# Kernel tuning notes

Measured on AMD Instinct MI355X. Metric: run time of the kernel, lower is better.

Reference implementation:

```python
import jax, jax.numpy as jnp
import numpy as np

B, R, C = 256, 1024, 1024
N_IDX = 64


def setup_inputs() -> dict:
    key = jax.random.key(0)
    kx, = jax.random.split(key, 1)
    x = jax.random.normal(kx, (B, R, C), dtype=jnp.float32)
    rows = jnp.arange(N_IDX, dtype=jnp.int32)
    cols = jnp.arange(N_IDX, dtype=jnp.int32)
    return {"x": x, "rows": rows, "cols": cols}


def _mute_msb(x):
    # frexp: x = m * 2**e with m in [0.5, 1). Muting the MSB of the exponent
    # (per the original: e = 0 if e > 0 else e) multiplies x by 2**(min(e,0)-e),
    # i.e. scales by 2**(-e) when e > 0, identity otherwise.
    e = jnp.frexp(x)[1]                                   # int exponent
    e = jax.lax.stop_gradient(e)
    scale = jnp.where(e > 0, jnp.exp2(-e.astype(x.dtype)), jnp.ones_like(x))
    return x * scale


def reference(x, rows, cols):
    # Boolean mask over the [R, C] plane selecting the (rows x cols) grid.
    mask = jnp.zeros((x.shape[1], x.shape[2]), dtype=bool)
    mask = mask.at[rows[:, None], cols[None, :]].set(True)
    y = _mute_msb(x)
    # Apply only on the selected grid, broadcast over batch.
    return jnp.where(mask[None, :, :], y, x)
```

## Files before the change

### kernel.cpp

```cpp
#include <hip/hip_runtime.h>
#include <hip/hip_bf16.h>


#define RR 1024
#define CC 1024
#define UNROLL 4

typedef float f4 __attribute__((ext_vector_type(4)));

__global__ void build_masks_kernel(const int* __restrict__ rows,
                                   const int* __restrict__ cols,
                                   unsigned* __restrict__ masks,
                                   int nr, int nc) {
    int t = threadIdx.x;
    if (t < 64) masks[t] = 0u;
    __syncthreads();
    if (t < nr) {
        int r = rows[t];
        atomicOr(&masks[r >> 5], 1u << (r & 31));
    }
    if (t < nc) {
        int c = cols[t];
        atomicOr(&masks[32 + (c >> 5)], 1u << (c & 31));
    }
}

__device__ __forceinline__ void mute4(f4& v, unsigned m) {
#pragma unroll
    for (int k = 0; k < 4; ++k) {
        if ((m >> k) & 1u) {
            unsigned u = __float_as_uint(v[k]);
            unsigned E = (u >> 23) & 0xffu;
            if (E >= 127u && E < 255u)
                v[k] = __uint_as_float((u & 0x807fffffu) | (126u << 23));
        }
    }
}

__global__ void copy_mute_kernel(const f4* __restrict__ x,
                                 f4* __restrict__ out,
                                 const unsigned* __restrict__ masks,
                                 int nrows) {
    __shared__ unsigned rowmask[32];
    int tid = threadIdx.x;
    if (tid < 32) rowmask[tid] = masks[tid];
    __syncthreads();

    unsigned colword = masks[32 + (tid >> 3)];
    unsigned colnib = (colword >> ((tid & 7) * 4)) & 0xFu;

    int rowstride = gridDim.x * UNROLL;
    long long qstride = (long long)rowstride * 256;

    int row = blockIdx.x * UNROLL;
    if (row >= nrows) return;
    long long q = (long long)row * 256 + tid;

    f4 v[UNROLL];
#pragma unroll
    for (int k = 0; k < UNROLL; ++k)
        v[k] = __builtin_nontemporal_load(&x[q + k * 256]);

    for (;;) {
        int nrow = row + rowstride;
        bool more = nrow < nrows;
        long long nq = q + qstride;

        f4 n[UNROLL];
        if (more) {
#pragma unroll
            for (int k = 0; k < UNROLL; ++k)
                n[k] = __builtin_nontemporal_load(&x[nq + k * 256]);
        }

#pragma unroll
        for (int k = 0; k < UNROLL; ++k) {
            int r = (row + k) & (RR - 1);
            unsigned m = ((rowmask[r >> 5] >> (r & 31)) & 1u) ? colnib : 0u;
            if (m) mute4(v[k], m);
            __builtin_nontemporal_store(v[k], &out[q + k * 256]);
        }

        if (!more) break;
#pragma unroll
        for (int k = 0; k < UNROLL; ++k) v[k] = n[k];
        row = nrow;
        q = nq;
    }
}

extern "C" void kernel_launch(void* const* d_in, const int* in_sizes, int n_in,
                              void* d_out, int out_size, void* d_ws, size_t ws_size,
                              hipStream_t stream) {
    const float* x  = (const float*)d_in[0];
    const int* rows = (const int*)d_in[1];
    const int* cols = (const int*)d_in[2];
    float* out      = (float*)d_out;
    unsigned* masks = (unsigned*)d_ws;

    const int nr = in_sizes[1];
    const int nc = in_sizes[2];

    build_masks_kernel<<<1, 64, 0, stream>>>(rows, cols, masks, nr, nc);

    int nrows = in_sizes[0] / CC;
    int block = 256;
    int grid = 4096;
    if (grid * UNROLL > nrows) grid = (nrows + UNROLL - 1) / UNROLL;
    copy_mute_kernel<<<grid, block, 0, stream>>>(
        (const f4*)x, (f4*)out, masks, nrows);
}
```

Measured before the change: 386.1 us.

## Fuse mask construction into copy kernel and double the per-thread unroll

Removes the separate one-block mask-building kernel. Each block of the copy kernel now builds the row and column bitmasks in shared memory from the index arrays, which saves a kernel launch and the dependency between the two kernels. UNROLL also goes from 4 to 8, so each thread keeps more 16-byte loads in flight and the grid gets smaller, and __launch_bounds__(256) is added. In exchange, every block repeats the small mask build with shared-memory atomics, register pressure rises, and the mask build assumes nr <= 64 and nc <= 192.

```diff
diff --git a/kernel.cpp b/kernel.cpp
--- a/kernel.cpp
+++ b/kernel.cpp
@@ -4,26 +4,9 @@
 
 #define RR 1024
 #define CC 1024
-#define UNROLL 4
+#define UNROLL 8
 
 typedef float f4 __attribute__((ext_vector_type(4)));
-
-__global__ void build_masks_kernel(const int* __restrict__ rows,
-                                   const int* __restrict__ cols,
-                                   unsigned* __restrict__ masks,
-                                   int nr, int nc) {
-    int t = threadIdx.x;
-    if (t < 64) masks[t] = 0u;
-    __syncthreads();
-    if (t < nr) {
-        int r = rows[t];
-        atomicOr(&masks[r >> 5], 1u << (r & 31));
-    }
-    if (t < nc) {
-        int c = cols[t];
-        atomicOr(&masks[32 + (c >> 5)], 1u << (c & 31));
-    }
-}
 
 __device__ __forceinline__ void mute4(f4& v, unsigned m) {
 #pragma unroll
@@ -37,16 +20,26 @@
     }
 }
 
-__global__ void copy_mute_kernel(const f4* __restrict__ x,
-                                 f4* __restrict__ out,
-                                 const unsigned* __restrict__ masks,
-                                 int nrows) {
-    __shared__ unsigned rowmask[32];
+__global__ void __launch_bounds__(256)
+copy_mute_kernel(const f4* __restrict__ x,
+                 f4* __restrict__ out,
+                 const int* __restrict__ rows,
+                 const int* __restrict__ cols,
+                 int nr, int nc, int nrows) {
+    __shared__ unsigned smask[64];
     int tid = threadIdx.x;
-    if (tid < 32) rowmask[tid] = masks[tid];
+    if (tid < 64) smask[tid] = 0u;
+    __syncthreads();
+    if (tid < nr) {
+        int r = rows[tid];
+        atomicOr(&smask[r >> 5], 1u << (r & 31));
+    } else if (tid >= 64 && tid < 64 + nc) {
+        int c = cols[tid - 64];
+        atomicOr(&smask[32 + (c >> 5)], 1u << (c & 31));
+    }
     __syncthreads();
 
-    unsigned colword = masks[32 + (tid >> 3)];
+    unsigned colword = smask[32 + (tid >> 3)];
     unsigned colnib = (colword >> ((tid & 7) * 4)) & 0xFu;
 
     int rowstride = gridDim.x * UNROLL;
@@ -76,7 +69,7 @@
 #pragma unroll
         for (int k = 0; k < UNROLL; ++k) {
             int r = (row + k) & (RR - 1);
-            unsigned m = ((rowmask[r >> 5] >> (r & 31)) & 1u) ? colnib : 0u;
+            unsigned m = ((smask[r >> 5] >> (r & 31)) & 1u) ? colnib : 0u;
             if (m) mute4(v[k], m);
             __builtin_nontemporal_store(v[k], &out[q + k * 256]);
         }
@@ -96,17 +89,14 @@
     const int* rows = (const int*)d_in[1];
     const int* cols = (const int*)d_in[2];
     float* out      = (float*)d_out;
-    unsigned* masks = (unsigned*)d_ws;
 
     const int nr = in_sizes[1];
     const int nc = in_sizes[2];
-
-    build_masks_kernel<<<1, 64, 0, stream>>>(rows, cols, masks, nr, nc);
 
     int nrows = in_sizes[0] / CC;
     int block = 256;
     int grid = 4096;
     if (grid * UNROLL > nrows) grid = (nrows + UNROLL - 1) / UNROLL;
     copy_mute_kernel<<<grid, block, 0, stream>>>(
-        (const f4*)x, (f4*)out, masks, nrows);
+        (const f4*)x, (f4*)out, rows, cols, nr, nc, nrows);
 }
```

After: 398.9 us. 3.3% more time.
